# Kernel tuning notes

Hardware: AMD Instinct MI355X
Metric: run time of the kernel (lower is better)

Reference implementation:

```python
import math
import jax, jax.numpy as jnp
import numpy as np

H = 16
D_MODEL = 1024
D_K = D_MODEL // H


def setup_inputs() -> dict:
    key = jax.random.key(0)
    ks = jax.random.split(key, 12)
    B, S = 4, 2048
    scale = 1.0 / math.sqrt(D_MODEL)
    inp = {
        "query": jax.random.normal(ks[0], (B, S, D_MODEL), jnp.float32),
        "key": jax.random.normal(ks[1], (B, S, D_MODEL), jnp.float32),
        "value": jax.random.normal(ks[2], (B, S, D_MODEL), jnp.float32),
        "mask": jnp.ones((B, 1, 1, S), jnp.int32),
        "Wq": jax.random.normal(ks[3], (D_MODEL, D_MODEL), jnp.float32) * scale,
        "bq": jnp.zeros((D_MODEL,), jnp.float32),
        "Wk": jax.random.normal(ks[4], (D_MODEL, D_MODEL), jnp.float32) * scale,
        "bk": jnp.zeros((D_MODEL,), jnp.float32),
        "Wv": jax.random.normal(ks[5], (D_MODEL, D_MODEL), jnp.float32) * scale,
        "bv": jnp.zeros((D_MODEL,), jnp.float32),
        "Wo": jax.random.normal(ks[6], (D_MODEL, D_MODEL), jnp.float32) * scale,
        "bo": jnp.zeros((D_MODEL,), jnp.float32),
    }
    return inp


def _split_heads(x, W, b):
    # x: (B, S, d_model) -> (B, H, S, d_k); torch Linear: x @ W.T + b
    B, S, _ = x.shape
    y = x @ W.T + b
    return y.reshape(B, S, H, D_K).transpose(0, 2, 1, 3)


def reference(query, key, value, mask, Wq, bq, Wk, bk, Wv, bv, Wo, bo):
    B, Sq, _ = query.shape
    q = _split_heads(query, Wq, bq)   # (B,H,Sq,dk)
    k = _split_heads(key, Wk, bk)     # (B,H,Skv,dk)
    v = _split_heads(value, Wv, bv)   # (B,H,Skv,dk)
    scores = jnp.einsum('bhqd,bhkd->bhqk', q, k) / math.sqrt(D_K)
    scores = jnp.where(mask == 0, jnp.float32(-1e9), scores)
    p_attn = jax.nn.softmax(scores, axis=-1)  # dropout p=0 (eval)
    x = jnp.einsum('bhqk,bhkd->bhqd', p_attn, v)
    x = x.transpose(0, 2, 1, 3).reshape(B, Sq, H * D_K)
    return x @ Wo.T + bo
```

## Files before the change

kernel.cpp:

```cpp
#include <hip/hip_runtime.h>
#include <hip/hip_bf16.h>
#include <stdint.h>

typedef unsigned short u16;
typedef short bf16x8 __attribute__((ext_vector_type(8)));
typedef float f32x4 __attribute__((ext_vector_type(4)));

#define D_MODEL 1024
#define NHEAD 16
#define DK 64
#define SEQ 2048
#define NB 4
#define MTOT (NB * SEQ)

__device__ __forceinline__ u16 f2bf(float f) {
  union { float f; unsigned u; } x; x.f = f;
  unsigned r = x.u + 0x7FFFu + ((x.u >> 16) & 1u);
  return (u16)(r >> 16);
}
#if __has_builtin(__builtin_amdgcn_cvt_pk_bf16_f32)
__device__ __forceinline__ unsigned pkbf(float a, float b) {
  auto r = __builtin_amdgcn_cvt_pk_bf16_f32(a, b);
  union { decltype(r) v; unsigned u; } c; c.v = r; return c.u;
}
#else
__device__ __forceinline__ unsigned pkbf(float a, float b) {
  return (unsigned)f2bf(a) | ((unsigned)f2bf(b) << 16);
}
#endif
#if __has_builtin(__builtin_amdgcn_exp2f)
__device__ __forceinline__ float exp2r(float x) { return __builtin_amdgcn_exp2f(x); }
#else
__device__ __forceinline__ float exp2r(float x) { return exp2f(x); }
#endif
__device__ __forceinline__ void gl_lds16(const u16* g, u16* s) {
  __builtin_amdgcn_global_load_lds(
      (const __attribute__((address_space(1))) void*)g,
      (__attribute__((address_space(3))) void*)s, 16, 0, 0);
}

struct CvtArgs {
  const float4* s[7];
  uint2* d[7];
  int n4[7];
};
__global__ __launch_bounds__(256) void cvt_all(CvtArgs a) {
  const int y = blockIdx.y;
  const float4* s = a.s[y];
  uint2* d = a.d[y];
  const int n4 = a.n4[y];
  for (int i = blockIdx.x * 256 + threadIdx.x; i < n4; i += gridDim.x * 256) {
    float4 x = s[i];
    uint2 o;
    o.x = pkbf(x.x, x.y);
    o.y = pkbf(x.z, x.w);
    d[i] = o;
  }
}

template <int MODE>
__device__ __forceinline__ void gemm_body(
    const u16* __restrict__ A, const u16* __restrict__ W,
    const float* __restrict__ bias, void* __restrict__ out, float scale,
    int m0, int n0, u16* smem)
{
  u16* As = smem;
  u16* Bs = smem + 8192;

  const int tid = threadIdx.x;
  const int l = tid & 63, w = tid >> 6;
  const int wm = (w >> 1) << 6, wn = (w & 1) << 6;

  int srow[4], sk8[4], sdst[4];
#pragma unroll
  for (int r = 0; r < 4; ++r) {
    int c = r * 256 + tid;
    srow[r] = c >> 3;
    sk8[r] = (c & 7) ^ (srow[r] & 7);
    sdst[r] = c << 3;
  }
  int aoff[4][2], boff[4][2];
#pragma unroll
  for (int i = 0; i < 4; ++i) {
    int mr = wm + (i << 4) + (l & 15);
    int nr = wn + (i << 4) + (l & 15);
#pragma unroll
    for (int s = 0; s < 2; ++s) {
      int kc = (s << 2) + (l >> 4);
      aoff[i][s] = (mr << 6) + ((kc ^ (mr & 7)) << 3);
      boff[i][s] = (nr << 6) + ((kc ^ (nr & 7)) << 3);
    }
  }

  const u16* Ab = A + (size_t)m0 * D_MODEL;
  const u16* Bb = W + (size_t)n0 * D_MODEL;

  f32x4 acc[4][4] = {};

  for (int kt = 0; kt < 16; ++kt) {
    const int kbase = kt << 6;
#pragma unroll
    for (int r = 0; r < 4; ++r)
      gl_lds16(Ab + (size_t)srow[r] * D_MODEL + kbase + (sk8[r] << 3), As + sdst[r]);
#pragma unroll
    for (int r = 0; r < 4; ++r)
      gl_lds16(Bb + (size_t)srow[r] * D_MODEL + kbase + (sk8[r] << 3), Bs + sdst[r]);
    __syncthreads();
#pragma unroll
    for (int s = 0; s < 2; ++s) {
      bf16x8 af[4], bfv[4];
#pragma unroll
      for (int i = 0; i < 4; ++i) af[i] = *(const bf16x8*)(As + aoff[i][s]);
#pragma unroll
      for (int j = 0; j < 4; ++j) bfv[j] = *(const bf16x8*)(Bs + boff[j][s]);
#pragma unroll
      for (int i = 0; i < 4; ++i)
#pragma unroll
        for (int j = 0; j < 4; ++j)
          acc[i][j] = __builtin_amdgcn_mfma_f32_16x16x32_bf16(af[i], bfv[j], acc[i][j], 0, 0, 0);
    }
    __syncthreads();
  }

  if (MODE == 1) {
    u16* Cs = smem;
    u16* outb = (u16*)out;
#pragma unroll
    for (int i = 0; i < 4; ++i)
#pragma unroll
      for (int j = 0; j < 4; ++j) {
        int sl = wm + (i << 4) + ((l >> 4) << 2);
        int nl = wn + (j << 4) + (l & 15);
        float bj = bias[n0 + nl];
        uint2 pk;
        pk.x = pkbf(acc[i][j][0] + bj, acc[i][j][1] + bj);
        pk.y = pkbf(acc[i][j][2] + bj, acc[i][j][3] + bj);
        *(uint2*)(Cs + nl * 136 + sl) = pk;
      }
    __syncthreads();
    int nl = tid >> 1, sh = (tid & 1) << 6;
    int n = n0 + nl;
    int b_ = m0 >> 11;
    const uint4* src = (const uint4*)(Cs + nl * 136 + sh);
    uint4* dst = (uint4*)(outb +
        (((size_t)b_ * NHEAD + (n >> 6)) * DK + (n & 63)) * SEQ + (m0 & 2047) + sh);
#pragma unroll
    for (int e = 0; e < 8; ++e) dst[e] = src[e];
  } else {
    u16* outb = (u16*)out;
    float* outf = (float*)out;
#pragma unroll
    for (int i = 0; i < 4; ++i)
#pragma unroll
      for (int j = 0; j < 4; ++j) {
        int ml = m0 + wm + (i << 4) + ((l >> 4) << 2);
        int n = n0 + wn + (j << 4) + (l & 15);
        float bj = bias[n];
#pragma unroll
        for (int r = 0; r < 4; ++r) {
          int m = ml + r;
          float v = (acc[i][j][r] + bj) * scale;
          if (MODE == 0)
            outb[(((size_t)(m >> 11) * NHEAD + (n >> 6)) * SEQ + (m & 2047)) * DK + (n & 63)] = f2bf(v);
          else
            outf[(size_t)m * D_MODEL + n] = v;
        }
      }
  }
}

template <int MODE>
__global__ __launch_bounds__(256) void gemm128(
    const u16* __restrict__ A, const u16* __restrict__ W,
    const float* __restrict__ bias, void* __restrict__ out, float scale)
{
  __shared__ alignas(16) u16 smem[17408];
  gemm_body<MODE>(A, W, bias, out, scale,
                  blockIdx.x << 7, blockIdx.y << 7, smem);
}

__global__ __launch_bounds__(256) void proj_qkv(
    const u16* __restrict__ Cq, const u16* __restrict__ Ck, const u16* __restrict__ Cv,
    const u16* __restrict__ wq, const u16* __restrict__ wk, const u16* __restrict__ wv,
    const float* __restrict__ bq, const float* __restrict__ bk, const float* __restrict__ bv,
    u16* __restrict__ Qb, u16* __restrict__ Kb, u16* __restrict__ Vt, float scq)
{
  __shared__ alignas(16) u16 smem[17408];
  const int z = blockIdx.z;
  const int m0 = blockIdx.x << 7, n0 = blockIdx.y << 7;
  if (z == 0)
    gemm_body<0>(Cq, wq, bq, Qb, scq, m0, n0, smem);
  else if (z == 1)
    gemm_body<0>(Ck, wk, bk, Kb, 1.0f, m0, n0, smem);
  else
    gemm_body<1>(Cv, wv, bv, Vt, 1.0f, m0, n0, smem);
}

__global__ __launch_bounds__(512, 4) void attn_fused(
    const u16* __restrict__ Q,
    const u16* __restrict__ K,
    const u16* __restrict__ Vt,
    const int* __restrict__ mask,
    u16* __restrict__ X)
{
  __shared__ alignas(16) u16 PQ[16384];
  __shared__ alignas(16) u16 Ks[2][4096];
  __shared__ alignas(16) u16 Vs[2][4096];
  __shared__ alignas(16) u16 On[1024];
  __shared__ alignas(16) float mbf[2][64];

  const int tid = threadIdx.x;
  const int l = tid & 63, w = tid >> 6;
  const int lq = l & 15, qd = l >> 4;
  const int bh = blockIdx.x;
  const int q0 = blockIdx.y << 8;
  const int b_ = bh >> 4, h = bh & 15;
  const size_t base = (size_t)bh * SEQ * DK;
  const int wq0 = w << 5;

#pragma unroll
  for (int r = 0; r < 4; ++r) {
    int c = r * 512 + tid;
    int row = c >> 3, k8 = (c & 7) ^ (row & 7);
    gl_lds16(Q + base + (size_t)(q0 + row) * DK + (k8 << 3), PQ + (c << 3));
  }
  if (tid < 256) {
    unsigned v = (tid < 16) ? 0x3F803F80u : 0u;
    uint2 pk; pk.x = v; pk.y = v;
    *(uint2*)(On + tid * 4) = pk;
  }
  {
    int row = tid >> 3, k8 = (tid & 7) ^ (row & 7);
    gl_lds16(K + base + (size_t)row * DK + (k8 << 3), Ks[0] + (tid << 3));
    gl_lds16(Vt + base + (size_t)row * SEQ + (k8 << 3), Vs[0] + (tid << 3));
  }
  if (tid < 64) mbf[0][tid] = mask[b_ * SEQ + tid] ? 0.0f : -1.44269504e9f;
  __syncthreads();

  bf16x8 qf[2][2];
#pragma unroll
  for (int i = 0; i < 2; ++i)
#pragma unroll
    for (int s = 0; s < 2; ++s) {
      int row = wq0 + (i << 4) + lq;
      qf[i][s] = *(const bf16x8*)(PQ + (row << 6) + ((((s << 2) + qd) ^ (row & 7)) << 3));
    }

  f32x4 Ov[2][4] = {};
  f32x4 Ovl[2] = {};

  for (int t = 0; t < 32; ++t) {
    const int cur = t & 1;
    if (t + 1 < 32) {
      const int kv1 = (t + 1) << 6;
      int row = tid >> 3, k8 = (tid & 7) ^ (row & 7);
      gl_lds16(K + base + (size_t)(kv1 + row) * DK + (k8 << 3), Ks[cur ^ 1] + (tid << 3));
      gl_lds16(Vt + base + (size_t)row * SEQ + kv1 + (k8 << 3), Vs[cur ^ 1] + (tid << 3));
      if (tid < 64) mbf[cur ^ 1][tid] = mask[b_ * SEQ + kv1 + tid] ? 0.0f : -1.44269504e9f;
    }

    float4 m4[4];
#pragma unroll
    for (int jb = 0; jb < 4; ++jb) m4[jb] = *(const float4*)(mbf[cur] + (jb << 4) + (qd << 2));

    f32x4 Sc[4][2];
#pragma unroll
    for (int jb = 0; jb < 4; ++jb)
#pragma unroll
      for (int i = 0; i < 2; ++i) {
        Sc[jb][i][0] = m4[jb].x; Sc[jb][i][1] = m4[jb].y;
        Sc[jb][i][2] = m4[jb].z; Sc[jb][i][3] = m4[jb].w;
      }
    const u16* Kc = Ks[cur];
    const u16* Vc = Vs[cur];
#pragma unroll
    for (int s = 0; s < 2; ++s) {
      bf16x8 kf[4];
#pragma unroll
      for (int jb = 0; jb < 4; ++jb) {
        int row = (jb << 4) + lq;
        kf[jb] = *(const bf16x8*)(Kc + (row << 6) + ((((s << 2) + qd) ^ (row & 7)) << 3));
      }
#pragma unroll
      for (int jb = 0; jb < 4; ++jb)
#pragma unroll
        for (int i = 0; i < 2; ++i)
          Sc[jb][i] = __builtin_amdgcn_mfma_f32_16x16x32_bf16(kf[jb], qf[i][s], Sc[jb][i], 0, 0, 0);
    }

#pragma unroll
    for (int i = 0; i < 2; ++i) {
      const int prow = wq0 + (i << 4) + lq;
      const int rbase = prow << 6;
      const int rsw = prow & 7;
#pragma unroll
      for (int jb = 0; jb < 4; ++jb) {
        float p0 = exp2r(Sc[jb][i][0]);
        float p1 = exp2r(Sc[jb][i][1]);
        float p2 = exp2r(Sc[jb][i][2]);
        float p3 = exp2r(Sc[jb][i][3]);
        uint2 pk;
        pk.x = pkbf(p0, p1);
        pk.y = pkbf(p2, p3);
        int c = (jb << 1) + (qd >> 1);
        *(uint2*)(PQ + rbase + ((c ^ rsw) << 3) + ((qd & 1) << 2)) = pk;
      }
    }

#pragma unroll
    for (int s = 0; s < 2; ++s) {
      bf16x8 pf[2], vf[4], vf1;
#pragma unroll
      for (int i = 0; i < 2; ++i) {
        int prow = wq0 + (i << 4) + lq;
        pf[i] = *(const bf16x8*)(PQ + (prow << 6) + ((((s << 2) + qd) ^ (prow & 7)) << 3));
      }
#pragma unroll
      for (int j = 0; j < 4; ++j) {
        int row = (j << 4) + lq;
        vf[j] = *(const bf16x8*)(Vc + (row << 6) + ((((s << 2) + qd) ^ (row & 7)) << 3));
      }
      vf1 = *(const bf16x8*)(On + (lq << 6) + ((((s << 2) + qd) ^ (lq & 7)) << 3));
#pragma unroll
      for (int i = 0; i < 2; ++i) {
#pragma unroll
        for (int j = 0; j < 4; ++j)
          Ov[i][j] = __builtin_amdgcn_mfma_f32_16x16x32_bf16(pf[i], vf[j], Ov[i][j], 0, 0, 0);
        Ovl[i] = __builtin_amdgcn_mfma_f32_16x16x32_bf16(pf[i], vf1, Ovl[i], 0, 0, 0);
      }
    }
    __syncthreads();
  }

#pragma unroll
  for (int i = 0; i < 2; ++i) {
    float inv[4];
#pragma unroll
    for (int r = 0; r < 4; ++r) inv[r] = 1.0f / Ovl[i][r];
#pragma unroll
    for (int r = 0; r < 4; ++r) {
      float sc_ = __shfl(inv[r], l & 48);
      int qrow = q0 + wq0 + (i << 4) + (qd << 2) + r;
#pragma unroll
      for (int j = 0; j < 4; ++j)
        X[((size_t)b_ * SEQ + qrow) * D_MODEL + (h << 6) + (j << 4) + lq] =
            f2bf(Ov[i][j][r] * sc_);
    }
  }
}

extern "C" void kernel_launch(void* const* d_in, const int* in_sizes, int n_in,
                              void* d_out, int out_size, void* d_ws, size_t ws_size,
                              hipStream_t stream) {
  const float* query = (const float*)d_in[0];
  const float* key_  = (const float*)d_in[1];
  const float* value = (const float*)d_in[2];
  const int* mask    = (const int*)d_in[3];
  const float* Wq = (const float*)d_in[4];
  const float* bq = (const float*)d_in[5];
  const float* Wk = (const float*)d_in[6];
  const float* bk = (const float*)d_in[7];
  const float* Wv = (const float*)d_in[8];
  const float* bv = (const float*)d_in[9];
  const float* Wo = (const float*)d_in[10];
  const float* bo = (const float*)d_in[11];

  u16* ws16 = (u16*)d_ws;
  const size_t WSZ = (size_t)D_MODEL * D_MODEL;
  const size_t ASZ = (size_t)MTOT * D_MODEL;
  const float SCQ = 0.125f * 1.44269504088896f;

  dim3 blk(256);
  dim3 gg(MTOT / 128, D_MODEL / 128);

  if (ws_size >= (size_t)(4 * WSZ + 4 * ASZ) * 2) {
    u16* wqc = ws16;
    u16* wkc = ws16 + WSZ;
    u16* wvc = ws16 + 2 * WSZ;
    u16* woc = ws16 + 3 * WSZ;
    u16* Cq  = ws16 + 4 * WSZ;
    u16* Ck  = ws16 + 4 * WSZ + ASZ;
    u16* Qb  = ws16 + 4 * WSZ + 2 * ASZ;
    u16* Kb  = ws16 + 4 * WSZ + 3 * ASZ;
    u16* Xb  = Cq;
    u16* Vtb = (u16*)d_out;
    u16* Cv  = (u16*)d_out + ASZ;

    CvtArgs ca;
    ca.s[0] = (const float4*)query; ca.d[0] = (uint2*)Cq;  ca.n4[0] = (int)(ASZ / 4);
    ca.s[1] = (const float4*)key_;  ca.d[1] = (uint2*)Ck;  ca.n4[1] = (int)(ASZ / 4);
    ca.s[2] = (const float4*)value; ca.d[2] = (uint2*)Cv;  ca.n4[2] = (int)(ASZ / 4);
    ca.s[3] = (const float4*)Wq;    ca.d[3] = (uint2*)wqc; ca.n4[3] = (int)(WSZ / 4);
    ca.s[4] = (const float4*)Wk;    ca.d[4] = (uint2*)wkc; ca.n4[4] = (int)(WSZ / 4);
    ca.s[5] = (const float4*)Wv;    ca.d[5] = (uint2*)wvc; ca.n4[5] = (int)(WSZ / 4);
    ca.s[6] = (const float4*)Wo;    ca.d[6] = (uint2*)woc; ca.n4[6] = (int)(WSZ / 4);

    cvt_all<<<dim3(512, 7), blk, 0, stream>>>(ca);
    proj_qkv<<<dim3(MTOT / 128, D_MODEL / 128, 3), blk, 0, stream>>>(
        Cq, Ck, Cv, wqc, wkc, wvc, bq, bk, bv, Qb, Kb, Vtb, SCQ);
    attn_fused<<<dim3(NB * NHEAD, SEQ / 256), dim3(512), 0, stream>>>(Qb, Kb, Vtb, mask, Xb);
    gemm128<2><<<gg, blk, 0, stream>>>(Xb, woc, bo, d_out, 1.0f);
  } else {
    u16* wqc = ws16;
    u16* wkc = ws16 + WSZ;
    u16* wvc = ws16 + 2 * WSZ;
    u16* woc = ws16 + 3 * WSZ;
    u16* C1  = ws16 + 4 * WSZ;
    u16* Qb  = ws16 + 4 * WSZ + ASZ;
    u16* Kb  = ws16 + 4 * WSZ + 2 * ASZ;
    u16* Xb  = C1;
    u16* Vtb = (u16*)d_out;

    CvtArgs cw;
    for (int i = 0; i < 7; ++i) { cw.s[i] = (const float4*)Wq; cw.d[i] = (uint2*)wqc; cw.n4[i] = 0; }
    cw.s[0] = (const float4*)Wq; cw.d[0] = (uint2*)wqc; cw.n4[0] = (int)(WSZ / 4);
    cw.s[1] = (const float4*)Wk; cw.d[1] = (uint2*)wkc; cw.n4[1] = (int)(WSZ / 4);
    cw.s[2] = (const float4*)Wv; cw.d[2] = (uint2*)wvc; cw.n4[2] = (int)(WSZ / 4);
    cw.s[3] = (const float4*)Wo; cw.d[3] = (uint2*)woc; cw.n4[3] = (int)(WSZ / 4);

    cvt_all<<<dim3(512, 4), blk, 0, stream>>>(cw);
    CvtArgs c1;
    c1.s[0] = (const float4*)query; c1.d[0] = (uint2*)C1; c1.n4[0] = (int)(ASZ / 4);
    cvt_all<<<dim3(1024, 1), blk, 0, stream>>>(c1);
    gemm128<0><<<gg, blk, 0, stream>>>(C1, wqc, bq, Qb, SCQ);
    c1.s[0] = (const float4*)key_;
    cvt_all<<<dim3(1024, 1), blk, 0, stream>>>(c1);
    gemm128<0><<<gg, blk, 0, stream>>>(C1, wkc, bk, Kb, 1.0f);
    c1.s[0] = (const float4*)value;
    cvt_all<<<dim3(1024, 1), blk, 0, stream>>>(c1);
    gemm128<1><<<gg, blk, 0, stream>>>(C1, wvc, bv, Vtb, 1.0f);
    attn_fused<<<dim3(NB * NHEAD, SEQ / 256), dim3(512), 0, stream>>>(Qb, Kb, Vtb, mask, Xb);
    gemm128<2><<<gg, blk, 0, stream>>>(Xb, woc, bo, d_out, 1.0f);
  }
}
```

Before: 335.8 us.

## Keep softmax probabilities in registers and widen attention warps to 64 query rows

The attention kernel now runs 256 threads per block, each wave handling 64 query rows instead of 32. The exponentiated scores are packed into bf16 MFMA operands directly in registers rather than written to and re-read from LDS. To match the accumulator layout, the V fragments are gathered as two 8-byte halves. The row-sum ones-vector moves from a shared buffer into a register constant. This removes the LDS round trip for P and halves K/V fragment reloads per query row, at the cost of more accumulator registers per thread and possibly lower occupancy.

```diff
diff --git a/kernel.cpp b/kernel.cpp
--- a/kernel.cpp
+++ b/kernel.cpp
@@ -196,7 +196,7 @@
     gemm_body<1>(Cv, wv, bv, Vt, 1.0f, m0, n0, smem);
 }
 
-__global__ __launch_bounds__(512, 4) void attn_fused(
+__global__ __launch_bounds__(256, 2) void attn_fused(
     const u16* __restrict__ Q,
     const u16* __restrict__ K,
     const u16* __restrict__ Vt,
@@ -206,7 +206,6 @@
   __shared__ alignas(16) u16 PQ[16384];
   __shared__ alignas(16) u16 Ks[2][4096];
   __shared__ alignas(16) u16 Vs[2][4096];
-  __shared__ alignas(16) u16 On[1024];
   __shared__ alignas(16) float mbf[2][64];
 
   const int tid = threadIdx.x;
@@ -216,124 +215,121 @@
   const int q0 = blockIdx.y << 8;
   const int b_ = bh >> 4, h = bh & 15;
   const size_t base = (size_t)bh * SEQ * DK;
-  const int wq0 = w << 5;
-
-#pragma unroll
-  for (int r = 0; r < 4; ++r) {
-    int c = r * 512 + tid;
+  const int wq0 = w << 6;
+
+#pragma unroll
+  for (int r = 0; r < 8; ++r) {
+    int c = r * 256 + tid;
     int row = c >> 3, k8 = (c & 7) ^ (row & 7);
     gl_lds16(Q + base + (size_t)(q0 + row) * DK + (k8 << 3), PQ + (c << 3));
   }
-  if (tid < 256) {
-    unsigned v = (tid < 16) ? 0x3F803F80u : 0u;
-    uint2 pk; pk.x = v; pk.y = v;
-    *(uint2*)(On + tid * 4) = pk;
-  }
-  {
-    int row = tid >> 3, k8 = (tid & 7) ^ (row & 7);
-    gl_lds16(K + base + (size_t)row * DK + (k8 << 3), Ks[0] + (tid << 3));
-    gl_lds16(Vt + base + (size_t)row * SEQ + (k8 << 3), Vs[0] + (tid << 3));
+#pragma unroll
+  for (int r = 0; r < 2; ++r) {
+    int c = r * 256 + tid;
+    int row = c >> 3, k8 = (c & 7) ^ (row & 7);
+    gl_lds16(K + base + (size_t)row * DK + (k8 << 3), Ks[0] + (c << 3));
+    gl_lds16(Vt + base + (size_t)row * SEQ + (k8 << 3), Vs[0] + (c << 3));
   }
   if (tid < 64) mbf[0][tid] = mask[b_ * SEQ + tid] ? 0.0f : -1.44269504e9f;
   __syncthreads();
 
-  bf16x8 qf[2][2];
-#pragma unroll
-  for (int i = 0; i < 2; ++i)
+  bf16x8 qf[4][2];
+#pragma unroll
+  for (int i = 0; i < 4; ++i)
 #pragma unroll
     for (int s = 0; s < 2; ++s) {
       int row = wq0 + (i << 4) + lq;
       qf[i][s] = *(const bf16x8*)(PQ + (row << 6) + ((((s << 2) + qd) ^ (row & 7)) << 3));
     }
 
-  f32x4 Ov[2][4] = {};
-  f32x4 Ovl[2] = {};
+  const short onev = (lq == 0) ? (short)0x3F80 : (short)0;
+  const bf16x8 onef = {onev, onev, onev, onev, onev, onev, onev, onev};
+
+  f32x4 Ov[4][4] = {};
+  f32x4 Ovl[4] = {};
 
   for (int t = 0; t < 32; ++t) {
     const int cur = t & 1;
     if (t + 1 < 32) {
       const int kv1 = (t + 1) << 6;
-      int row = tid >> 3, k8 = (tid & 7) ^ (row & 7);
-      gl_lds16(K + base + (size_t)(kv1 + row) * DK + (k8 << 3), Ks[cur ^ 1] + (tid << 3));
-      gl_lds16(Vt + base + (size_t)row * SEQ + kv1 + (k8 << 3), Vs[cur ^ 1] + (tid << 3));
+#pragma unroll
+      for (int r = 0; r < 2; ++r) {
+        int c = r * 256 + tid;
+        int row = c >> 3, k8 = (c & 7) ^ (row & 7);
+        gl_lds16(K + base + (size_t)(kv1 + row) * DK + (k8 << 3), Ks[cur ^ 1] + (c << 3));
+        gl_lds16(Vt + base + (size_t)row * SEQ + kv1 + (k8 << 3), Vs[cur ^ 1] + (c << 3));
+      }
       if (tid < 64) mbf[cur ^ 1][tid] = mask[b_ * SEQ + kv1 + tid] ? 0.0f : -1.44269504e9f;
     }
 
-    float4 m4[4];
-#pragma unroll
-    for (int jb = 0; jb < 4; ++jb) m4[jb] = *(const float4*)(mbf[cur] + (jb << 4) + (qd << 2));
-
-    f32x4 Sc[4][2];
-#pragma unroll
-    for (int jb = 0; jb < 4; ++jb)
-#pragma unroll
-      for (int i = 0; i < 2; ++i) {
-        Sc[jb][i][0] = m4[jb].x; Sc[jb][i][1] = m4[jb].y;
-        Sc[jb][i][2] = m4[jb].z; Sc[jb][i][3] = m4[jb].w;
-      }
     const u16* Kc = Ks[cur];
     const u16* Vc = Vs[cur];
-#pragma unroll
-    for (int s = 0; s < 2; ++s) {
-      bf16x8 kf[4];
+
+    bf16x8 kf[2][4];
+#pragma unroll
+    for (int s = 0; s < 2; ++s)
 #pragma unroll
       for (int jb = 0; jb < 4; ++jb) {
         int row = (jb << 4) + lq;
-        kf[jb] = *(const bf16x8*)(Kc + (row << 6) + ((((s << 2) + qd) ^ (row & 7)) << 3));
-      }
-#pragma unroll
-      for (int jb = 0; jb < 4; ++jb)
-#pragma unroll
-        for (int i = 0; i < 2; ++i)
-          Sc[jb][i] = __builtin_amdgcn_mfma_f32_16x16x32_bf16(kf[jb], qf[i][s], Sc[jb][i], 0, 0, 0);
-    }
-
-#pragma unroll
-    for (int i = 0; i < 2; ++i) {
-      const int prow = wq0 + (i << 4) + lq;
-      const int rbase = prow << 6;
-      const int rsw = prow & 7;
-#pragma unroll
-      for (int jb = 0; jb < 4; ++jb) {
-        float p0 = exp2r(Sc[jb][i][0]);
-        float p1 = exp2r(Sc[jb][i][1]);
-        float p2 = exp2r(Sc[jb][i][2]);
-        float p3 = exp2r(Sc[jb][i][3]);
-        uint2 pk;
-        pk.x = pkbf(p0, p1);
-        pk.y = pkbf(p2, p3);
-        int c = (jb << 1) + (qd >> 1);
-        *(uint2*)(PQ + rbase + ((c ^ rsw) << 3) + ((qd & 1) << 2)) = pk;
-      }
-    }
-
-#pragma unroll
-    for (int s = 0; s < 2; ++s) {
-      bf16x8 pf[2], vf[4], vf1;
-#pragma unroll
-      for (int i = 0; i < 2; ++i) {
-        int prow = wq0 + (i << 4) + lq;
-        pf[i] = *(const bf16x8*)(PQ + (prow << 6) + ((((s << 2) + qd) ^ (prow & 7)) << 3));
-      }
+        kf[s][jb] = *(const bf16x8*)(Kc + (row << 6) + ((((s << 2) + qd) ^ (row & 7)) << 3));
+      }
+
+    bf16x8 vfv[2][4];
+#pragma unroll
+    for (int s = 0; s < 2; ++s)
 #pragma unroll
       for (int j = 0; j < 4; ++j) {
         int row = (j << 4) + lq;
-        vf[j] = *(const bf16x8*)(Vc + (row << 6) + ((((s << 2) + qd) ^ (row & 7)) << 3));
-      }
-      vf1 = *(const bf16x8*)(On + (lq << 6) + ((((s << 2) + qd) ^ (lq & 7)) << 3));
-#pragma unroll
-      for (int i = 0; i < 2; ++i) {
+        int rsw = row & 7;
+        uint2 c0 = *(const uint2*)(Vc + (row << 6) +
+                    ((((s << 2) + (qd >> 1)) ^ rsw) << 3) + ((qd & 1) << 2));
+        uint2 c1 = *(const uint2*)(Vc + (row << 6) +
+                    ((((s << 2) + 2 + (qd >> 1)) ^ rsw) << 3) + ((qd & 1) << 2));
+        union { uint4 u; bf16x8 v; } cv;
+        cv.u.x = c0.x; cv.u.y = c0.y; cv.u.z = c1.x; cv.u.w = c1.y;
+        vfv[s][j] = cv.v;
+      }
+
+    float4 m4[4];
+#pragma unroll
+    for (int jb = 0; jb < 4; ++jb) m4[jb] = *(const float4*)(mbf[cur] + (jb << 4) + (qd << 2));
+
+#pragma unroll
+    for (int i = 0; i < 4; ++i) {
+      f32x4 Sc[4];
+#pragma unroll
+      for (int jb = 0; jb < 4; ++jb) {
+        Sc[jb][0] = m4[jb].x; Sc[jb][1] = m4[jb].y;
+        Sc[jb][2] = m4[jb].z; Sc[jb][3] = m4[jb].w;
+      }
+#pragma unroll
+      for (int s = 0; s < 2; ++s)
+#pragma unroll
+        for (int jb = 0; jb < 4; ++jb)
+          Sc[jb] = __builtin_amdgcn_mfma_f32_16x16x32_bf16(kf[s][jb], qf[i][s], Sc[jb], 0, 0, 0);
+
+      unsigned pkv[4][2];
+#pragma unroll
+      for (int jb = 0; jb < 4; ++jb) {
+        pkv[jb][0] = pkbf(exp2r(Sc[jb][0]), exp2r(Sc[jb][1]));
+        pkv[jb][1] = pkbf(exp2r(Sc[jb][2]), exp2r(Sc[jb][3]));
+      }
+#pragma unroll
+      for (int s = 0; s < 2; ++s) {
+        union { uint4 u; bf16x8 v; } pfu;
+        pfu.u.x = pkv[2 * s][0];     pfu.u.y = pkv[2 * s][1];
+        pfu.u.z = pkv[2 * s + 1][0]; pfu.u.w = pkv[2 * s + 1][1];
 #pragma unroll
         for (int j = 0; j < 4; ++j)
-          Ov[i][j] = __builtin_amdgcn_mfma_f32_16x16x32_bf16(pf[i], vf[j], Ov[i][j], 0, 0, 0);
-        Ovl[i] = __builtin_amdgcn_mfma_f32_16x16x32_bf16(pf[i], vf1, Ovl[i], 0, 0, 0);
+          Ov[i][j] = __builtin_amdgcn_mfma_f32_16x16x32_bf16(pfu.v, vfv[s][j], Ov[i][j], 0, 0, 0);
+        Ovl[i] = __builtin_amdgcn_mfma_f32_16x16x32_bf16(pfu.v, onef, Ovl[i], 0, 0, 0);
       }
     }
     __syncthreads();
   }
 
 #pragma unroll
-  for (int i = 0; i < 2; ++i) {
+  for (int i = 0; i < 4; ++i) {
     float inv[4];
 #pragma unroll
     for (int r = 0; r < 4; ++r) inv[r] = 1.0f / Ovl[i][r];
@@ -398,7 +394,7 @@
     cvt_all<<<dim3(512, 7), blk, 0, stream>>>(ca);
     proj_qkv<<<dim3(MTOT / 128, D_MODEL / 128, 3), blk, 0, stream>>>(
         Cq, Ck, Cv, wqc, wkc, wvc, bq, bk, bv, Qb, Kb, Vtb, SCQ);
-    attn_fused<<<dim3(NB * NHEAD, SEQ / 256), dim3(512), 0, stream>>>(Qb, Kb, Vtb, mask, Xb);
+    attn_fused<<<dim3(NB * NHEAD, SEQ / 256), blk, 0, stream>>>(Qb, Kb, Vtb, mask, Xb);
     gemm128<2><<<gg, blk, 0, stream>>>(Xb, woc, bo, d_out, 1.0f);
   } else {
     u16* wqc = ws16;
@@ -429,7 +425,7 @@
     c1.s[0] = (const float4*)value;
     cvt_all<<<dim3(1024, 1), blk, 0, stream>>>(c1);
     gemm128<1><<<gg, blk, 0, stream>>>(C1, wvc, bv, Vtb, 1.0f);
-    attn_fused<<<dim3(NB * NHEAD, SEQ / 256), dim3(512), 0, stream>>>(Qb, Kb, Vtb, mask, Xb);
+    attn_fused<<<dim3(NB * NHEAD, SEQ / 256), blk, 0, stream>>>(Qb, Kb, Vtb, mask, Xb);
     gemm128<2><<<gg, blk, 0, stream>>>(Xb, woc, bo, d_out, 1.0f);
   }
 }
```

Result: slower. 344.2 us (+2.5%).
